# Optimization experiments

Hardware: AMD Instinct MI355X
Metric: run time of the kernel (lower is better)

## Reference

```python
import jax, jax.numpy as jnp
import numpy as np

B, S, D_IN, D_OUT = 4, 2048, 4096, 11008


def setup_inputs() -> dict:
    key = jax.random.key(0)
    kx, kw, ks, kb = jax.random.split(key, 4)
    x = jax.random.normal(kx, (B, S, D_IN), dtype=jnp.float32)
    # Simulate fp8 storage: values are exactly representable in float8_e4m3fn.
    w_raw = jax.random.normal(kw, (D_OUT, D_IN), dtype=jnp.float32)
    w_q = w_raw.astype(jnp.float8_e4m3fn).astype(jnp.float32)
    # Per-output-channel dequant scale (positive).
    scale = jax.random.uniform(ks, (D_OUT, 1), dtype=jnp.float32, minval=0.01, maxval=0.1)
    bias = jax.random.normal(kb, (D_OUT,), dtype=jnp.float32)
    return {"x": x, "w_q": w_q, "scale": scale, "bias": bias}


def reference(x, w_q, scale, bias):
    # dequantize_tensor: fp8 payload * per-channel scale -> full-precision weight [D_OUT, D_IN]
    w = w_q * scale
    # F.linear(x, w, bias) = x @ w.T + bias
    out = jnp.einsum('bsd,od->bso', x, w) + bias
    return out
```

## Files before the change

kernel.cpp:

```cpp
#include <hip/hip_runtime.h>
#include <hip/hip_bf16.h>
#include <stdint.h>

#define M_DIM 8192
#define N_DIM 11008
#define K_DIM 4096
#define BM 256
#define BN 256
#define BK 32
#define NT (K_DIM / BK)
#define TSLOT (BM * BK)
#define NBX (N_DIM / BN)
#define NBY (M_DIM / BM)
#define NBLK (NBX * NBY)
#define CPX (NBLK / 8)

typedef __bf16 bf16_8 __attribute__((ext_vector_type(8)));
typedef float f32x4 __attribute__((ext_vector_type(4)));

__device__ __forceinline__ uint32_t pack_bf2(float lo, float hi) {
    uint32_t ulo = __float_as_uint(lo);
    uint32_t uhi = __float_as_uint(hi);
    ulo = (ulo + 0x7fffu + ((ulo >> 16) & 1u)) >> 16;
    uhi = (uhi + 0x7fffu + ((uhi >> 16) & 1u)) >> 16;
    return ulo | (uhi << 16);
}

__global__ __launch_bounds__(256) void cvt_f32_bf16(const float* __restrict__ src,
                                                    uint2* __restrict__ dst, int n4) {
    int i = blockIdx.x * 256 + threadIdx.x;
    if (i >= n4) return;
    float4 a = ((const float4*)src)[i];
    uint2 o;
    o.x = pack_bf2(a.x, a.y);
    o.y = pack_bf2(a.z, a.w);
    dst[i] = o;
}

__device__ __forceinline__ void load_lds16(const __bf16* g, __bf16* l) {
    __builtin_amdgcn_global_load_lds(
        (__attribute__((address_space(1))) void*)(g),
        (__attribute__((address_space(3))) void*)(l),
        16, 0, 0);
}

#define VMCNT(n) asm volatile("s_waitcnt vmcnt(" #n ")" ::: "memory")
#define LGKM(n)  asm volatile("s_waitcnt lgkmcnt(" #n ")" ::: "memory")
#define SCHED0   __builtin_amdgcn_sched_barrier(0)

__device__ __forceinline__ void wg_barrier() {
    asm volatile("" ::: "memory");
    __builtin_amdgcn_s_barrier();
    asm volatile("" ::: "memory");
}

__device__ __forceinline__ void stage_pair(const __bf16* G, __bf16* L, int wave, long ko) {
    __bf16* lw = L + wave * 16 * BK;
    load_lds16(G + ko, lw);
    load_lds16(G + 128L * K_DIM + ko, lw + 128 * BK);
}

template <bool HAS_NEXT>
__device__ __forceinline__ void kstep(
    int tt, const __bf16* AsB, const __bf16* BsB, __bf16* AsW, __bf16* BsW,
    int aoff, int boff, const __bf16* Ag, const __bf16* Wg, int wave,
    bf16_8 (&a0)[4], bf16_8 (&bv)[4],
    bf16_8 (&a0n)[4], bf16_8 (&bvn)[4],
    bf16_8 (&a1)[4],
    f32x4 (&acc)[8][4]) {
    const int sl = tt & 3;
    const __bf16* Ab = AsB + sl * TSLOT + aoff;
    const __bf16* Bb = BsB + sl * TSLOT + boff;
    const bool doStage = (tt + 3) < NT;
    const int sn = (tt + 3) & 3;
    const long ko = (long)(tt + 3) * BK;

    if (doStage) stage_pair(Ag, AsW + sn * TSLOT, wave, ko);
#pragma unroll
    for (int i = 0; i < 4; i++) a1[i] = *(const bf16_8*)(Ab + (4 + i) * 16 * BK);
    wg_barrier();
    LGKM(4);
    SCHED0;
    __builtin_amdgcn_s_setprio(1);
#pragma unroll
    for (int i = 0; i < 4; i++)
#pragma unroll
        for (int j = 0; j < 4; j++)
            acc[i][j] = __builtin_amdgcn_mfma_f32_16x16x32_bf16(a0[i], bv[j], acc[i][j], 0, 0, 0);
    __builtin_amdgcn_s_setprio(0);

    if (doStage) stage_pair(Wg, BsW + sn * TSLOT, wave, ko);
    if (HAS_NEXT) {
        const int sl1 = (tt + 1) & 3;
        const __bf16* Abn = AsB + sl1 * TSLOT + aoff;
        const __bf16* Bbn = BsB + sl1 * TSLOT + boff;
#pragma unroll
        for (int i = 0; i < 4; i++) a0n[i] = *(const bf16_8*)(Abn + i * 16 * BK);
#pragma unroll
        for (int j = 0; j < 4; j++) bvn[j] = *(const bf16_8*)(Bbn + j * 16 * BK);
        LGKM(8);
    } else {
        LGKM(0);
    }
    SCHED0;
    __builtin_amdgcn_s_setprio(1);
#pragma unroll
    for (int i = 0; i < 4; i++)
#pragma unroll
        for (int j = 0; j < 4; j++)
            acc[4 + i][j] = __builtin_amdgcn_mfma_f32_16x16x32_bf16(a1[i], bv[j], acc[4 + i][j], 0, 0, 0);
    __builtin_amdgcn_s_setprio(0);

    if (tt < NT - 3) { VMCNT(4); }
    else if (tt == NT - 3) { VMCNT(0); }
    wg_barrier();
}

__global__ __launch_bounds__(512, 2) void gemm_bt_scaled(
    const __bf16* __restrict__ A, const __bf16* __restrict__ W,
    const float* __restrict__ scale, const float* __restrict__ bias,
    float* __restrict__ C) {
    __shared__ __align__(16) __bf16 As[4][TSLOT];
    __shared__ __align__(16) __bf16 Bs[4][TSLOT];

    const int t = threadIdx.x;
    const int wave = t >> 6;
    const int lane = t & 63;
    const int wm = wave >> 2;
    const int wn = wave & 3;

    const int bid = (int)blockIdx.x;
    const int swz = (bid & 7) * CPX + (bid >> 3);
    const int by = swz / NBX;
    const int bx = swz - by * NBX;
    const int m0 = by * BM;
    const int n0 = bx * BN;

    const int srow = lane >> 2;
    const int sch = ((lane & 3) ^ ((lane >> 3) & 3)) * 8;
    const __bf16* Ag = A + (long)(m0 + wave * 16 + srow) * K_DIM + sch;
    const __bf16* Wg = W + (long)(n0 + wave * 16 + srow) * K_DIM + sch;

    const int lrow = lane & 15;
    const int swzr = (lrow >> 1) & 3;
    const int lk = ((lane >> 4) ^ swzr) * 8;
    const int aoff = (wm * 128 + lrow) * BK + lk;
    const int boff = (wn * 64 + lrow) * BK + lk;

    const __bf16* AsB = &As[0][0];
    const __bf16* BsB = &Bs[0][0];
    __bf16* AsW = &As[0][0];
    __bf16* BsW = &Bs[0][0];

    f32x4 acc[8][4] = {};
    bf16_8 a0A[4], bvA[4], a0B[4], bvB[4], a1[4];

    stage_pair(Ag, AsW + 0 * TSLOT, wave, 0);
    stage_pair(Wg, BsW + 0 * TSLOT, wave, 0);
    stage_pair(Ag, AsW + 1 * TSLOT, wave, (long)BK);
    stage_pair(Wg, BsW + 1 * TSLOT, wave, (long)BK);
    stage_pair(Ag, AsW + 2 * TSLOT, wave, 2L * BK);
    stage_pair(Wg, BsW + 2 * TSLOT, wave, 2L * BK);
    VMCNT(8);
    wg_barrier();
#pragma unroll
    for (int i = 0; i < 4; i++) a0A[i] = *(const bf16_8*)(AsB + aoff + i * 16 * BK);
#pragma unroll
    for (int j = 0; j < 4; j++) bvA[j] = *(const bf16_8*)(BsB + boff + j * 16 * BK);

    int tt = 0;
#pragma unroll 1
    for (int it = 0; it < (NT - 2) / 2; ++it) {
        kstep<true>(tt, AsB, BsB, AsW, BsW, aoff, boff, Ag, Wg, wave,
                    a0A, bvA, a0B, bvB, a1, acc);
        ++tt;
        kstep<true>(tt, AsB, BsB, AsW, BsW, aoff, boff, Ag, Wg, wave,
                    a0B, bvB, a0A, bvA, a1, acc);
        ++tt;
    }
    kstep<true>(tt, AsB, BsB, AsW, BsW, aoff, boff, Ag, Wg, wave,
                a0A, bvA, a0B, bvB, a1, acc);
    ++tt;
    kstep<false>(tt, AsB, BsB, AsW, BsW, aoff, boff, Ag, Wg, wave,
                 a0B, bvB, a0A, bvA, a1, acc);

    const int crow4 = (lane >> 4) * 4;
    const int ccol = lane & 15;
#pragma unroll
    for (int j = 0; j < 4; j++) {
        const int n = n0 + wn * 64 + j * 16 + ccol;
        const float sc = scale[n];
        const float bi = bias[n];
#pragma unroll
        for (int i = 0; i < 8; i++) {
            const int mbase = m0 + wm * 128 + i * 16 + crow4;
#pragma unroll
            for (int r = 0; r < 4; r++) {
                C[(long)(mbase + r) * N_DIM + n] = acc[i][j][r] * sc + bi;
            }
        }
    }
}

extern "C" void kernel_launch(void* const* d_in, const int* in_sizes, int n_in,
                              void* d_out, int out_size, void* d_ws, size_t ws_size,
                              hipStream_t stream) {
    const float* x = (const float*)d_in[0];
    const float* w_q = (const float*)d_in[1];
    const float* scale = (const float*)d_in[2];
    const float* bias = (const float*)d_in[3];
    float* out = (float*)d_out;

    __bf16* x_bf = (__bf16*)d_ws;
    __bf16* w_bf = (__bf16*)((char*)d_ws + (size_t)M_DIM * K_DIM * sizeof(__bf16));

    const int n4x = (M_DIM * K_DIM) / 4;
    const int n4w = (N_DIM * K_DIM) / 4;
    cvt_f32_bf16<<<(n4x + 255) / 256, 256, 0, stream>>>(x, (uint2*)x_bf, n4x);
    cvt_f32_bf16<<<(n4w + 255) / 256, 256, 0, stream>>>(w_q, (uint2*)w_bf, n4w);

    gemm_bt_scaled<<<dim3(NBLK), 512, 0, stream>>>(x_bf, w_bf, scale, bias, out);
}
```

Baseline: 1.418 ms.

## Prepack weights into MFMA fragment layout and load B directly to registers

Adds a weight conversion kernel that writes bf16 weights in a per-16-column, per-k-step fragment order. The GEMM then loads B fragments straight from global memory into registers with one-step prefetch, and only A is staged through LDS. This halves LDS use and removes the B staging and its LDS reads. In exchange, B loads are duplicated across the M-waves and carry global-memory latency, and the pipeline's wait counts were rewritten.

```diff
diff --git a/kernel.cpp b/kernel.cpp
--- a/kernel.cpp
+++ b/kernel.cpp
@@ -9,7 +9,8 @@
 #define BN 256
 #define BK 32
 #define NT (K_DIM / BK)
-#define TSLOT (BM * BK)
+#define NKS NT
+#define ASLOT (BM * BK)
 #define NBX (N_DIM / BN)
 #define NBY (M_DIM / BM)
 #define NBLK (NBX * NBY)
@@ -37,6 +38,32 @@
     dst[i] = o;
 }
 
+__global__ __launch_bounds__(256) void cvt_w_pack(const float* __restrict__ W,
+                                                  __bf16* __restrict__ Wp) {
+    __shared__ __bf16 lds[16][136];
+    const int jt = blockIdx.x;
+    const int kg = blockIdx.y;
+    const int tid = threadIdx.x;
+    const int r = tid >> 4;
+    const int c = tid & 15;
+    const float* src = W + (long)(jt * 16 + r) * K_DIM + kg * 128 + c * 8;
+    float4 f0 = ((const float4*)src)[0];
+    float4 f1 = ((const float4*)src)[1];
+    uint4 pk;
+    pk.x = pack_bf2(f0.x, f0.y);
+    pk.y = pack_bf2(f0.z, f0.w);
+    pk.z = pack_bf2(f1.x, f1.y);
+    pk.w = pack_bf2(f1.z, f1.w);
+    *(uint4*)&lds[r][c * 8] = pk;
+    __syncthreads();
+    const int ksl = tid >> 6;
+    const int lane = tid & 63;
+    const int rr = lane & 15;
+    const int p = lane >> 4;
+    uint4 v = *(const uint4*)&lds[rr][ksl * 32 + p * 8];
+    ((uint4*)Wp)[(long)((jt * NKS) + kg * 4 + ksl) * 64 + lane] = v;
+}
+
 __device__ __forceinline__ void load_lds16(const __bf16* g, __bf16* l) {
     __builtin_amdgcn_global_load_lds(
         (__attribute__((address_space(1))) void*)(g),
@@ -54,31 +81,34 @@
     asm volatile("" ::: "memory");
 }
 
-__device__ __forceinline__ void stage_pair(const __bf16* G, __bf16* L, int wave, long ko) {
+__device__ __forceinline__ void stage_A(const __bf16* Ag, __bf16* L, int wave, long ko) {
     __bf16* lw = L + wave * 16 * BK;
-    load_lds16(G + ko, lw);
-    load_lds16(G + 128L * K_DIM + ko, lw + 128 * BK);
-}
-
-template <bool HAS_NEXT>
+    load_lds16(Ag + ko, lw);
+    load_lds16(Ag + 128L * K_DIM + ko, lw + 128 * BK);
+}
+
+template <bool STAGE, bool BPRE, bool APRE, int VM>
 __device__ __forceinline__ void kstep(
-    int tt, const __bf16* AsB, const __bf16* BsB, __bf16* AsW, __bf16* BsW,
-    int aoff, int boff, const __bf16* Ag, const __bf16* Wg, int wave,
-    bf16_8 (&a0)[4], bf16_8 (&bv)[4],
-    bf16_8 (&a0n)[4], bf16_8 (&bvn)[4],
+    int tt, const __bf16* AsB, __bf16* AsW, int aoff,
+    const __bf16* Ag, int wave, const __bf16* Bp,
+    bf16_8 (&a0)[4], bf16_8 (&a0n)[4],
+    bf16_8 (&bv)[4], bf16_8 (&bvn)[4],
     bf16_8 (&a1)[4],
     f32x4 (&acc)[8][4]) {
-    const int sl = tt & 3;
-    const __bf16* Ab = AsB + sl * TSLOT + aoff;
-    const __bf16* Bb = BsB + sl * TSLOT + boff;
-    const bool doStage = (tt + 3) < NT;
-    const int sn = (tt + 3) & 3;
-    const long ko = (long)(tt + 3) * BK;
-
-    if (doStage) stage_pair(Ag, AsW + sn * TSLOT, wave, ko);
+    if (STAGE) {
+        stage_A(Ag, AsW + ((tt + 3) & 3) * ASLOT, wave, (long)(tt + 3) * BK);
+    }
+    if (BPRE) {
+#pragma unroll
+        for (int j = 0; j < 4; j++)
+            bvn[j] = *(const bf16_8*)(Bp + (long)(j * NKS + (tt + 1)) * 512);
+    }
+    const __bf16* Ab = AsB + (tt & 3) * ASLOT + aoff;
 #pragma unroll
     for (int i = 0; i < 4; i++) a1[i] = *(const bf16_8*)(Ab + (4 + i) * 16 * BK);
-    wg_barrier();
+    if constexpr (VM == 6) VMCNT(6);
+    else if constexpr (VM == 4) VMCNT(4);
+    else VMCNT(0);
     LGKM(4);
     SCHED0;
     __builtin_amdgcn_s_setprio(1);
@@ -88,17 +118,11 @@
         for (int j = 0; j < 4; j++)
             acc[i][j] = __builtin_amdgcn_mfma_f32_16x16x32_bf16(a0[i], bv[j], acc[i][j], 0, 0, 0);
     __builtin_amdgcn_s_setprio(0);
-
-    if (doStage) stage_pair(Wg, BsW + sn * TSLOT, wave, ko);
-    if (HAS_NEXT) {
-        const int sl1 = (tt + 1) & 3;
-        const __bf16* Abn = AsB + sl1 * TSLOT + aoff;
-        const __bf16* Bbn = BsB + sl1 * TSLOT + boff;
+    if (APRE) {
+        const __bf16* Abn = AsB + ((tt + 1) & 3) * ASLOT + aoff;
 #pragma unroll
         for (int i = 0; i < 4; i++) a0n[i] = *(const bf16_8*)(Abn + i * 16 * BK);
-#pragma unroll
-        for (int j = 0; j < 4; j++) bvn[j] = *(const bf16_8*)(Bbn + j * 16 * BK);
-        LGKM(8);
+        LGKM(4);
     } else {
         LGKM(0);
     }
@@ -110,18 +134,14 @@
         for (int j = 0; j < 4; j++)
             acc[4 + i][j] = __builtin_amdgcn_mfma_f32_16x16x32_bf16(a1[i], bv[j], acc[4 + i][j], 0, 0, 0);
     __builtin_amdgcn_s_setprio(0);
-
-    if (tt < NT - 3) { VMCNT(4); }
-    else if (tt == NT - 3) { VMCNT(0); }
-    wg_barrier();
+    if (STAGE || BPRE) wg_barrier();
 }
 
 __global__ __launch_bounds__(512, 2) void gemm_bt_scaled(
-    const __bf16* __restrict__ A, const __bf16* __restrict__ W,
+    const __bf16* __restrict__ A, const __bf16* __restrict__ Wp,
     const float* __restrict__ scale, const float* __restrict__ bias,
     float* __restrict__ C) {
-    __shared__ __align__(16) __bf16 As[4][TSLOT];
-    __shared__ __align__(16) __bf16 Bs[4][TSLOT];
+    __shared__ __align__(16) __bf16 As[4][ASLOT];
 
     const int t = threadIdx.x;
     const int wave = t >> 6;
@@ -139,50 +159,53 @@
     const int srow = lane >> 2;
     const int sch = ((lane & 3) ^ ((lane >> 3) & 3)) * 8;
     const __bf16* Ag = A + (long)(m0 + wave * 16 + srow) * K_DIM + sch;
-    const __bf16* Wg = W + (long)(n0 + wave * 16 + srow) * K_DIM + sch;
 
     const int lrow = lane & 15;
     const int swzr = (lrow >> 1) & 3;
     const int lk = ((lane >> 4) ^ swzr) * 8;
     const int aoff = (wm * 128 + lrow) * BK + lk;
-    const int boff = (wn * 64 + lrow) * BK + lk;
+
+    const int jt0 = n0 / 16 + wn * 4;
+    const __bf16* Bp = Wp + (long)jt0 * NKS * 512 + lane * 8;
 
     const __bf16* AsB = &As[0][0];
-    const __bf16* BsB = &Bs[0][0];
     __bf16* AsW = &As[0][0];
-    __bf16* BsW = &Bs[0][0];
 
     f32x4 acc[8][4] = {};
-    bf16_8 a0A[4], bvA[4], a0B[4], bvB[4], a1[4];
-
-    stage_pair(Ag, AsW + 0 * TSLOT, wave, 0);
-    stage_pair(Wg, BsW + 0 * TSLOT, wave, 0);
-    stage_pair(Ag, AsW + 1 * TSLOT, wave, (long)BK);
-    stage_pair(Wg, BsW + 1 * TSLOT, wave, (long)BK);
-    stage_pair(Ag, AsW + 2 * TSLOT, wave, 2L * BK);
-    stage_pair(Wg, BsW + 2 * TSLOT, wave, 2L * BK);
-    VMCNT(8);
+    bf16_8 a0A[4], a0B[4], bvA[4], bvB[4], a1[4];
+
+    stage_A(Ag, AsW + 0 * ASLOT, wave, 0);
+    stage_A(Ag, AsW + 1 * ASLOT, wave, (long)BK);
+    stage_A(Ag, AsW + 2 * ASLOT, wave, 2L * BK);
+#pragma unroll
+    for (int j = 0; j < 4; j++)
+        bvA[j] = *(const bf16_8*)(Bp + (long)(j * NKS) * 512);
+    VMCNT(4);
     wg_barrier();
 #pragma unroll
     for (int i = 0; i < 4; i++) a0A[i] = *(const bf16_8*)(AsB + aoff + i * 16 * BK);
-#pragma unroll
-    for (int j = 0; j < 4; j++) bvA[j] = *(const bf16_8*)(BsB + boff + j * 16 * BK);
 
     int tt = 0;
 #pragma unroll 1
-    for (int it = 0; it < (NT - 2) / 2; ++it) {
-        kstep<true>(tt, AsB, BsB, AsW, BsW, aoff, boff, Ag, Wg, wave,
-                    a0A, bvA, a0B, bvB, a1, acc);
+    for (int it = 0; it < 62; ++it) {
+        kstep<true, true, true, 6>(tt, AsB, AsW, aoff, Ag, wave, Bp,
+                                   a0A, a0B, bvA, bvB, a1, acc);
         ++tt;
-        kstep<true>(tt, AsB, BsB, AsW, BsW, aoff, boff, Ag, Wg, wave,
-                    a0B, bvB, a0A, bvA, a1, acc);
+        kstep<true, true, true, 6>(tt, AsB, AsW, aoff, Ag, wave, Bp,
+                                   a0B, a0A, bvB, bvA, a1, acc);
         ++tt;
     }
-    kstep<true>(tt, AsB, BsB, AsW, BsW, aoff, boff, Ag, Wg, wave,
-                a0A, bvA, a0B, bvB, a1, acc);
+    kstep<true, true, true, 6>(tt, AsB, AsW, aoff, Ag, wave, Bp,
+                               a0A, a0B, bvA, bvB, a1, acc);
     ++tt;
-    kstep<false>(tt, AsB, BsB, AsW, BsW, aoff, boff, Ag, Wg, wave,
-                 a0B, bvB, a0A, bvA, a1, acc);
+    kstep<false, true, true, 4>(tt, AsB, AsW, aoff, Ag, wave, Bp,
+                                a0B, a0A, bvB, bvA, a1, acc);
+    ++tt;
+    kstep<false, true, true, 4>(tt, AsB, AsW, aoff, Ag, wave, Bp,
+                                a0A, a0B, bvA, bvB, a1, acc);
+    ++tt;
+    kstep<false, false, false, 0>(tt, AsB, AsW, aoff, Ag, wave, Bp,
+                                  a0B, a0A, bvB, bvA, a1, acc);
 
     const int crow4 = (lane >> 4) * 4;
     const int ccol = lane & 15;
@@ -212,12 +235,11 @@
     float* out = (float*)d_out;
 
     __bf16* x_bf = (__bf16*)d_ws;
-    __bf16* w_bf = (__bf16*)((char*)d_ws + (size_t)M_DIM * K_DIM * sizeof(__bf16));
+    __bf16* w_pk = (__bf16*)((char*)d_ws + (size_t)M_DIM * K_DIM * sizeof(__bf16));
 
     const int n4x = (M_DIM * K_DIM) / 4;
-    const int n4w = (N_DIM * K_DIM) / 4;
     cvt_f32_bf16<<<(n4x + 255) / 256, 256, 0, stream>>>(x, (uint2*)x_bf, n4x);
-    cvt_f32_bf16<<<(n4w + 255) / 256, 256, 0, stream>>>(w_q, (uint2*)w_bf, n4w);
-
-    gemm_bt_scaled<<<dim3(NBLK), 512, 0, stream>>>(x_bf, w_bf, scale, bias, out);
-}
+    cvt_w_pack<<<dim3(N_DIM / 16, K_DIM / 128), 256, 0, stream>>>(w_q, w_pk);
+
+    gemm_bt_scaled<<<dim3(NBLK), 512, 0, stream>>>(x_bf, w_pk, scale, bias, out);
+}
```

Result: faster. 1.339 ms (-5.6%).
